# Kernel optimization log

Hardware: AMD Instinct MI355X
Metric: run time of the kernel (lower is better)

The kernel has to match this reference:

```python
import jax, jax.numpy as jnp
import numpy as np

B, T, D = 4, 2048, 1024

def setup_inputs() -> dict:
    key = jax.random.key(0)
    kx, kq, kk, kv = jax.random.split(key, 4)
    scale = 1.0 / np.sqrt(D)
    return {
        "x": jax.random.normal(kx, (B, T, D), dtype=jnp.float32),
        "Wq": jax.random.normal(kq, (D, D), dtype=jnp.float32) * scale,
        "Wk": jax.random.normal(kk, (D, D), dtype=jnp.float32) * scale,
        "Wv": jax.random.normal(kv, (D, D), dtype=jnp.float32) * scale,
    }

def reference(x, Wq, Wk, Wv):
    # torch Linear: y = x @ W.T (no bias, qkv_bias=False)
    q = jnp.einsum("btd,od->bto", x, Wq)
    k = jnp.einsum("btd,od->bto", x, Wk)
    v = jnp.einsum("btd,od->bto", x, Wv)
    scores = jnp.einsum("bqd,bkd->bqk", q, k)
    # NOTE: source uses non-in-place masked_fill whose result is discarded,
    # so NO causal mask is actually applied. Faithfully reproduced here.
    inv_sqrt_d = 1.0 / np.sqrt(k.shape[-1]).astype(np.float32)
    weights = jax.nn.softmax(scores * inv_sqrt_d, axis=-1)
    # dropout p=0.0 -> identity
    return jnp.einsum("bqk,bkd->bqd", weights, v)
```

## Files before the change

### kernel.cpp

```cpp
#include <hip/hip_runtime.h>
#include <hip/hip_bf16.h>
#include <hip/hip_fp16.h>
#include <type_traits>

typedef _Float16 f16;
typedef __attribute__((ext_vector_type(8))) _Float16 f16x8;
typedef __attribute__((ext_vector_type(4))) float floatx4;

#define B_ 4
#define T_ 2048
#define D_ 1024

#define XB_OFF   0ul
#define WB_OFF   16777216ul
#define QKV_OFF  23068672ul
#define S_OFF    73400320ul
#define VT_OFF   0ul

#define ASYNC16(gp, lp) \
    __builtin_amdgcn_global_load_lds((const __attribute__((address_space(1))) unsigned int*)(gp), \
                                     (__attribute__((address_space(3))) unsigned int*)(lp), 16, 0, 0)

__global__ __launch_bounds__(256) void cast_all(
    const float* __restrict__ x, const float* __restrict__ wq,
    const float* __restrict__ wk, const float* __restrict__ wv,
    f16* __restrict__ xb, f16* __restrict__ wb)
{
    long i = (long)blockIdx.x * 256 + threadIdx.x;
    const float4* src; f16* dst;
    if (i < 2097152L)            { src = (const float4*)x;  dst = xb; }
    else if (i < 2359296L)       { i -= 2097152L; src = (const float4*)wq; dst = wb; }
    else if (i < 2621440L)       { i -= 2359296L; src = (const float4*)wk; dst = wb + 1048576; }
    else                         { i -= 2621440L; src = (const float4*)wv; dst = wb + 2097152; }
    float4 v = src[i];
    union { f16 h[4]; uint2 u; } o;
    o.h[0] = (f16)v.x; o.h[1] = (f16)v.y; o.h[2] = (f16)v.z; o.h[3] = (f16)v.w;
    ((uint2*)dst)[i] = o.u;
}

template <typename CT, int BN, int WN>
__global__ __launch_bounds__(256, 2) void gemm_nt(
    const f16* __restrict__ A, int lda, long sA,
    const f16* __restrict__ B, int ldb, long sB,
    CT* __restrict__ C, int ldc, long sC,
    int K, float alpha)
{
    __shared__ f16 As[2][128 * 32];
    __shared__ f16 Bs[2][BN * 32];

    const int tid = threadIdx.x;
    const int m0 = blockIdx.y * 128;
    const int n0 = blockIdx.x * BN;
    const int bz = blockIdx.z;
    A += (long)bz * sA;
    B += (long)bz * sB;
    C += (long)bz * sC;

    const int w  = tid >> 6;
    const int l  = tid & 63;
    const int wm = (w >> 1) * 64;
    const int wn = (w & 1) * WN;
    const int lr = l & 15;
    const int kg = l >> 4;
    const int kx = kg ^ ((lr >> 1) & 3);

    constexpr int NI = WN / 16;
    floatx4 acc[4][NI] = {};

    const int srow = tid >> 2;
    const int gsl  = (tid & 3) ^ ((tid >> 3) & 3);
    const long ldaL = lda, ldbL = ldb;
    const f16* Aptr = A + (long)(m0 + srow) * ldaL + gsl * 8;
    const f16* Bptr = B + (long)(n0 + srow) * ldbL + gsl * 8;

    auto stage = [&](int b, int kk) {
        #pragma unroll
        for (int rh = 0; rh < 2; rh++)
            ASYNC16(Aptr + kk + rh * 64 * ldaL, &As[b][rh * 2048 + w * 512]);
        #pragma unroll
        for (int rh = 0; rh < BN / 64; rh++)
            ASYNC16(Bptr + kk + rh * 64 * ldbL, &Bs[b][rh * 2048 + w * 512]);
    };

    stage(0, 0);
    __syncthreads();

    for (int k0 = 0; k0 < K; k0 += 32) {
        const int cur = (k0 >> 5) & 1;
        if (k0 + 32 < K) stage(cur ^ 1, k0 + 32);

        f16x8 af[4], bf[NI];
        #pragma unroll
        for (int mi = 0; mi < 4; mi++)
            af[mi] = *(const f16x8*)&As[cur][(wm + mi * 16 + lr) * 32 + kx * 8];
        #pragma unroll
        for (int ni = 0; ni < NI; ni++)
            bf[ni] = *(const f16x8*)&Bs[cur][(wn + ni * 16 + lr) * 32 + kx * 8];
        #pragma unroll
        for (int mi = 0; mi < 4; mi++)
            #pragma unroll
            for (int ni = 0; ni < NI; ni++)
                acc[mi][ni] = __builtin_amdgcn_mfma_f32_16x16x32_f16(af[mi], bf[ni], acc[mi][ni], 0, 0, 0);

        __syncthreads();
    }

    #pragma unroll
    for (int mi = 0; mi < 4; mi++) {
        #pragma unroll
        for (int ni = 0; ni < NI; ni++) {
            #pragma unroll
            for (int r = 0; r < 4; r++) {
                int row = m0 + wm + mi * 16 + kg * 4 + r;
                int col = n0 + wn + ni * 16 + lr;
                float v = acc[mi][ni][r] * alpha;
                if constexpr (std::is_same<CT, float>::value)
                    C[(long)row * ldc + col] = v;
                else
                    C[(long)row * ldc + col] = (f16)v;
            }
        }
    }
}

__global__ __launch_bounds__(256) void transpose_v(const f16* __restrict__ qkv, f16* __restrict__ vt)
{
    __shared__ f16 tile[32][33];
    int b  = blockIdx.z;
    int j0 = blockIdx.x * 32;
    int d0 = blockIdx.y * 32;
    int tx = threadIdx.x & 31;
    int ty = threadIdx.x >> 5;
    #pragma unroll
    for (int i = 0; i < 4; i++) {
        int j = j0 + ty + i * 8;
        tile[ty + i * 8][tx] = qkv[((long)b * T_ + j) * 3072 + 2048 + d0 + tx];
    }
    __syncthreads();
    #pragma unroll
    for (int i = 0; i < 4; i++) {
        int d = d0 + ty + i * 8;
        vt[((long)b * D_ + d) * T_ + j0 + tx] = tile[tx][ty + i * 8];
    }
}

__global__ __launch_bounds__(256) void softmax_rows(f16* __restrict__ S)
{
    long row = (long)blockIdx.x * 4 + (threadIdx.x >> 6);
    int l = threadIdx.x & 63;
    uint4* p4 = (uint4*)(S + row * 2048);
    union U { uint4 u; f16 h[8]; } d[4];
    float v[32];
    float mx = -1e30f;
    #pragma unroll
    for (int i = 0; i < 4; i++) {
        d[i].u = p4[i * 64 + l];
        #pragma unroll
        for (int j = 0; j < 8; j++) { v[i * 8 + j] = (float)d[i].h[j]; mx = fmaxf(mx, v[i * 8 + j]); }
    }
    #pragma unroll
    for (int off = 32; off; off >>= 1) mx = fmaxf(mx, __shfl_xor(mx, off, 64));
    float s = 0.f;
    #pragma unroll
    for (int i = 0; i < 32; i++) { v[i] = __expf(v[i] - mx); s += v[i]; }
    #pragma unroll
    for (int off = 32; off; off >>= 1) s += __shfl_xor(s, off, 64);
    float inv = 1.f / s;
    #pragma unroll
    for (int i = 0; i < 4; i++) {
        #pragma unroll
        for (int j = 0; j < 8; j++) d[i].h[j] = (f16)(v[i * 8 + j] * inv);
        p4[i * 64 + l] = d[i].u;
    }
}

extern "C" void kernel_launch(void* const* d_in, const int* in_sizes, int n_in,
                              void* d_out, int out_size, void* d_ws, size_t ws_size,
                              hipStream_t stream)
{
    const float* x  = (const float*)d_in[0];
    const float* wq = (const float*)d_in[1];
    const float* wk = (const float*)d_in[2];
    const float* wv = (const float*)d_in[3];
    float* out = (float*)d_out;
    char* ws = (char*)d_ws;
    f16* xb  = (f16*)(ws + XB_OFF);
    f16* wb  = (f16*)(ws + WB_OFF);
    f16* qkv = (f16*)(ws + QKV_OFF);
    f16* s   = (f16*)(ws + S_OFF);
    f16* vt  = (f16*)(ws + VT_OFF);

    cast_all<<<11264, 256, 0, stream>>>(x, wq, wk, wv, xb, wb);

    gemm_nt<f16, 256, 128><<<dim3(12, 64, 1), 256, 0, stream>>>(
        xb, 1024, 0L, wb, 1024, 0L, qkv, 3072, 0L, 1024, 1.0f);

    transpose_v<<<dim3(64, 32, 4), 256, 0, stream>>>(qkv, vt);

    gemm_nt<f16, 256, 128><<<dim3(8, 16, 4), 256, 0, stream>>>(
        qkv,        3072, (long)T_ * 3072,
        qkv + 1024, 3072, (long)T_ * 3072,
        s,          2048, (long)T_ * 2048, 1024, 0.03125f);

    softmax_rows<<<2048, 256, 0, stream>>>(s);

    gemm_nt<float, 128, 64><<<dim3(8, 16, 4), 256, 0, stream>>>(
        s,  2048, (long)T_ * 2048,
        vt, 2048, (long)D_ * 2048,
        out, 1024, (long)T_ * 1024, 2048, 1.0f);
}
```

Baseline: 278.3 us.

## Rewrite GEMM with per-wave private LDS B tiles and direct global A loads

The shared GEMM kernel is restructured so that each wave stages only its own 64-row slice of B into a private LDS region. A fragments are loaded straight from global memory into registers and double-buffered, which removes all block-wide barriers from the K loop. Every call now uses a uniform 128x128 tile with K as a template constant, and the grids grow accordingly. The cost is lost LDS sharing of A across waves, so global traffic goes up, and correctness now depends on a manual waitcnt to order the async LDS loads.

```diff
diff --git a/kernel.cpp b/kernel.cpp
--- a/kernel.cpp
+++ b/kernel.cpp
@@ -38,19 +38,18 @@
     ((uint2*)dst)[i] = o.u;
 }
 
-template <typename CT, int BN, int WN>
-__global__ __launch_bounds__(256, 2) void gemm_nt(
+template <typename CT, int K>
+__global__ __launch_bounds__(256) void gemm_nt(
     const f16* __restrict__ A, int lda, long sA,
     const f16* __restrict__ B, int ldb, long sB,
     CT* __restrict__ C, int ldc, long sC,
-    int K, float alpha)
-{
-    __shared__ f16 As[2][128 * 32];
-    __shared__ f16 Bs[2][BN * 32];
+    float alpha)
+{
+    __shared__ f16 Bs[4][2][2048];
 
     const int tid = threadIdx.x;
     const int m0 = blockIdx.y * 128;
-    const int n0 = blockIdx.x * BN;
+    const int n0 = blockIdx.x * 128;
     const int bz = blockIdx.z;
     A += (long)bz * sA;
     B += (long)bz * sB;
@@ -59,56 +58,61 @@
     const int w  = tid >> 6;
     const int l  = tid & 63;
     const int wm = (w >> 1) * 64;
-    const int wn = (w & 1) * WN;
+    const int wn = (w & 1) * 64;
     const int lr = l & 15;
     const int kg = l >> 4;
     const int kx = kg ^ ((lr >> 1) & 3);
 
-    constexpr int NI = WN / 16;
-    floatx4 acc[4][NI] = {};
-
-    const int srow = tid >> 2;
-    const int gsl  = (tid & 3) ^ ((tid >> 3) & 3);
+    floatx4 acc[4][4] = {};
+
     const long ldaL = lda, ldbL = ldb;
-    const f16* Aptr = A + (long)(m0 + srow) * ldaL + gsl * 8;
-    const f16* Bptr = B + (long)(n0 + srow) * ldbL + gsl * 8;
-
-    auto stage = [&](int b, int kk) {
-        #pragma unroll
-        for (int rh = 0; rh < 2; rh++)
-            ASYNC16(Aptr + kk + rh * 64 * ldaL, &As[b][rh * 2048 + w * 512]);
-        #pragma unroll
-        for (int rh = 0; rh < BN / 64; rh++)
-            ASYNC16(Bptr + kk + rh * 64 * ldbL, &Bs[b][rh * 2048 + w * 512]);
+    const int gsl = (l & 3) ^ ((l >> 3) & 3);
+    const f16* Bl  = B + (long)(n0 + wn + (l >> 2)) * ldbL + gsl * 8;
+    const f16* Alp = A + (long)(m0 + wm + lr) * ldaL + kg * 8;
+
+    auto stageB = [&](int buf, int kk) {
+        #pragma unroll
+        for (int c = 0; c < 4; c++)
+            ASYNC16(Bl + kk + c * 16 * ldbL, &Bs[w][buf][c * 512]);
     };
-
-    stage(0, 0);
-    __syncthreads();
-
+    auto loadA = [&](f16x8* af, int kk) {
+        #pragma unroll
+        for (int mi = 0; mi < 4; mi++)
+            af[mi] = *(const f16x8*)(Alp + kk + (long)(mi * 16) * ldaL);
+    };
+
+    f16x8 afc[4], afn[4];
+    stageB(0, 0);
+    loadA(afc, 0);
+
+    #pragma unroll 2
     for (int k0 = 0; k0 < K; k0 += 32) {
-        const int cur = (k0 >> 5) & 1;
-        if (k0 + 32 < K) stage(cur ^ 1, k0 + 32);
-
-        f16x8 af[4], bf[NI];
-        #pragma unroll
-        for (int mi = 0; mi < 4; mi++)
-            af[mi] = *(const f16x8*)&As[cur][(wm + mi * 16 + lr) * 32 + kx * 8];
-        #pragma unroll
-        for (int ni = 0; ni < NI; ni++)
-            bf[ni] = *(const f16x8*)&Bs[cur][(wn + ni * 16 + lr) * 32 + kx * 8];
+        const int buf = (k0 >> 5) & 1;
+        if (k0 + 32 < K) {
+            stageB(buf ^ 1, k0 + 32);
+            loadA(afn, k0 + 32);
+        }
+
+        __builtin_amdgcn_s_waitcnt(0xF7C);
+
+        f16x8 bf[4];
+        #pragma unroll
+        for (int ni = 0; ni < 4; ni++)
+            bf[ni] = *(const f16x8*)&Bs[w][buf][(ni * 16 + lr) * 32 + kx * 8];
         #pragma unroll
         for (int mi = 0; mi < 4; mi++)
             #pragma unroll
-            for (int ni = 0; ni < NI; ni++)
-                acc[mi][ni] = __builtin_amdgcn_mfma_f32_16x16x32_f16(af[mi], bf[ni], acc[mi][ni], 0, 0, 0);
-
-        __syncthreads();
+            for (int ni = 0; ni < 4; ni++)
+                acc[mi][ni] = __builtin_amdgcn_mfma_f32_16x16x32_f16(afc[mi], bf[ni], acc[mi][ni], 0, 0, 0);
+
+        #pragma unroll
+        for (int mi = 0; mi < 4; mi++) afc[mi] = afn[mi];
     }
 
     #pragma unroll
     for (int mi = 0; mi < 4; mi++) {
         #pragma unroll
-        for (int ni = 0; ni < NI; ni++) {
+        for (int ni = 0; ni < 4; ni++) {
             #pragma unroll
             for (int r = 0; r < 4; r++) {
                 int row = m0 + wm + mi * 16 + kg * 4 + r;
@@ -192,20 +196,20 @@
 
     cast_all<<<11264, 256, 0, stream>>>(x, wq, wk, wv, xb, wb);
 
-    gemm_nt<f16, 256, 128><<<dim3(12, 64, 1), 256, 0, stream>>>(
-        xb, 1024, 0L, wb, 1024, 0L, qkv, 3072, 0L, 1024, 1.0f);
+    gemm_nt<f16, 1024><<<dim3(24, 64, 1), 256, 0, stream>>>(
+        xb, 1024, 0L, wb, 1024, 0L, qkv, 3072, 0L, 1.0f);
 
     transpose_v<<<dim3(64, 32, 4), 256, 0, stream>>>(qkv, vt);
 
-    gemm_nt<f16, 256, 128><<<dim3(8, 16, 4), 256, 0, stream>>>(
+    gemm_nt<f16, 1024><<<dim3(16, 16, 4), 256, 0, stream>>>(
         qkv,        3072, (long)T_ * 3072,
         qkv + 1024, 3072, (long)T_ * 3072,
-        s,          2048, (long)T_ * 2048, 1024, 0.03125f);
+        s,          2048, (long)T_ * 2048, 0.03125f);
 
     softmax_rows<<<2048, 256, 0, stream>>>(s);
 
-    gemm_nt<float, 128, 64><<<dim3(8, 16, 4), 256, 0, stream>>>(
+    gemm_nt<float, 2048><<<dim3(8, 16, 4), 256, 0, stream>>>(
         s,  2048, (long)T_ * 2048,
         vt, 2048, (long)D_ * 2048,
-        out, 1024, (long)T_ * 1024, 2048, 1.0f);
-}
+        out, 1024, (long)T_ * 1024, 1.0f);
+}
```

New measurement: 395.2 us. 42.0% more time.
